# Performance work log

Hardware: AMD Instinct MI355X
Metric: run time of the kernel (lower is better)

## Reference

```python
import jax, jax.numpy as jnp
import numpy as np


def setup_inputs() -> dict:
    key = jax.random.key(0)
    k1, k2 = jax.random.split(key)
    z_e_x = jax.random.normal(k1, (4096, 16, 128), dtype=jnp.float32)
    codebook = jax.random.normal(k2, (1024, 128), dtype=jnp.float32)
    return {"z_e_x": z_e_x, "codebook": codebook}


def reference(z_e_x, codebook):
    # VQStraightThrough.forward: nearest-codebook quantization in fp32.
    B, N, C = z_e_x.shape
    x = z_e_x.astype(jnp.float32).reshape(B * N, C)          # [BN, C]
    cb = codebook.astype(jnp.float32)                        # [K, C]
    inputs_sq = jnp.sum(x * x, axis=1, keepdims=True)        # [BN, 1]
    codebook_sq = jnp.sum(cb * cb, axis=1)                   # [K]
    l2_dis = inputs_sq + codebook_sq - 2.0 * (x @ cb.T)      # [BN, K]
    flat_idx = jnp.argmin(l2_dis, axis=1)                    # [BN] int
    min_vals = jnp.min(l2_dis, axis=1)                       # [BN]
    idx = flat_idx.reshape(B, N)
    distances = min_vals.reshape(B, N).astype(z_e_x.dtype)
    codes = cb[flat_idx].reshape(B, N, C).astype(z_e_x.dtype)  # gather
    return codes, flat_idx, idx, distances
```

## Files before the change

### kernel.cpp

```cpp
#include <hip/hip_runtime.h>
#include <math.h>
#include <stdint.h>

#define C        128
#define KCODES   1024
#define TPB      256
#define ROWS_PB  128
#define NCHUNK   64
#define NCHUNKS  (KCODES / NCHUNK)
#define BSTRIDE  272
#define EPS_TRIG 0.25f

typedef __attribute__((ext_vector_type(8))) short bf16x8_t;
typedef __attribute__((ext_vector_type(4))) float f32x4_t;

static __device__ __forceinline__ uint32_t bf16_rne(float f) {
    uint32_t u = __float_as_uint(f);
    return (u + 0x7FFFu + ((u >> 16) & 1u)) >> 16;
}
static __device__ __forceinline__ float bf16_hi_f(float f) {
    return __uint_as_float(bf16_rne(f) << 16);
}

__global__ void cb_split_kernel(const float* __restrict__ cb,
                                uint16_t* __restrict__ cbh,
                                uint16_t* __restrict__ cbl) {
    int i = blockIdx.x * blockDim.x + threadIdx.x;
    if (i >= KCODES * C) return;
    float f = cb[i];
    uint32_t h = bf16_rne(f);
    float lo = f - __uint_as_float(h << 16);
    cbh[i] = (uint16_t)h;
    cbl[i] = (uint16_t)bf16_rne(lo);
}

__global__ void cbsq_kernel(const float* __restrict__ cb, float* __restrict__ cbsq) {
    const int k = blockIdx.x * blockDim.x + threadIdx.x;
    if (k >= KCODES) return;
    const float4* cp = (const float4*)(cb + (size_t)k * C);
    float sx = 0.f, sy = 0.f, sz = 0.f, sw = 0.f;
    #pragma unroll
    for (int i = 0; i < C / 4; ++i) {
        float4 v = cp[i];
        sx += v.x * v.x; sy += v.y * v.y;
        sz += v.z * v.z; sw += v.w * v.w;
    }
    cbsq[k] = (sx + sy) + (sz + sw);
}

#define SLOTS(OP) OP(0,0) OP(0,1) OP(0,2) OP(0,3) OP(1,0) OP(1,1) OP(1,2) OP(1,3)
#define MFMA_BF16 __builtin_amdgcn_mfma_f32_16x16x32_bf16

__global__ __launch_bounds__(TPB, 3)
void vq_mfma_kernel(const float* __restrict__ x,
                    const float* __restrict__ cb,
                    const uint16_t* __restrict__ cbh,
                    const uint16_t* __restrict__ cbl,
                    const float* __restrict__ cq,
                    float* __restrict__ out_codes,
                    float* __restrict__ out_fidx,
                    float* __restrict__ out_idx,
                    float* __restrict__ out_dist,
                    int rows)
{
    __shared__ __align__(16) uint8_t s_buf[NCHUNK * 2 * BSTRIDE];
    __shared__ float s_cq[NCHUNK];
    __shared__ float s_v1[ROWS_PB], s_v2[ROWS_PB];
    __shared__ int   s_k1[ROWS_PB], s_k2[ROWS_PB];

    const int t    = threadIdx.x;
    const int lane = t & 63;
    const int w    = t >> 6;
    const int ln   = lane & 15;
    const int quad = lane >> 4;
    const int rowblock = blockIdx.x * ROWS_PB;

    #pragma unroll 4
    for (int i = 0; i < 16; ++i) {
        int fid = t + i * TPB;
        int row = fid >> 5;
        int kq  = fid & 31;
        int grow = rowblock + row;
        grow = grow < rows ? grow : rows - 1;
        float4 v = ((const float4*)x)[(size_t)grow * 32 + kq];
        uint32_t p0 = bf16_rne(v.x) | (bf16_rne(v.y) << 16);
        uint32_t p1 = bf16_rne(v.z) | (bf16_rne(v.w) << 16);
        *(uint2*)(s_buf + row * BSTRIDE + kq * 8) = make_uint2(p0, p1);
    }
    __syncthreads();

    const int arow0 = (w * 32 + ln) * BSTRIDE;
    const int arow1 = (w * 32 + 16 + ln) * BSTRIDE;
    bf16x8_t ah00, ah01, ah02, ah03, ah10, ah11, ah12, ah13;
    ah00 = *(const bf16x8_t*)(s_buf + arow0 + 0 * 64 + quad * 16);
    ah01 = *(const bf16x8_t*)(s_buf + arow0 + 1 * 64 + quad * 16);
    ah02 = *(const bf16x8_t*)(s_buf + arow0 + 2 * 64 + quad * 16);
    ah03 = *(const bf16x8_t*)(s_buf + arow0 + 3 * 64 + quad * 16);
    ah10 = *(const bf16x8_t*)(s_buf + arow1 + 0 * 64 + quad * 16);
    ah11 = *(const bf16x8_t*)(s_buf + arow1 + 1 * 64 + quad * 16);
    ah12 = *(const bf16x8_t*)(s_buf + arow1 + 2 * 64 + quad * 16);
    ah13 = *(const bf16x8_t*)(s_buf + arow1 + 3 * 64 + quad * 16);
    __syncthreads();

    #pragma unroll 4
    for (int i = 0; i < 16; ++i) {
        int fid = t + i * TPB;
        int row = fid >> 5;
        int kq  = fid & 31;
        int grow = rowblock + row;
        grow = grow < rows ? grow : rows - 1;
        float4 v = ((const float4*)x)[(size_t)grow * 32 + kq];
        uint32_t p0 = bf16_rne(v.x - bf16_hi_f(v.x)) | (bf16_rne(v.y - bf16_hi_f(v.y)) << 16);
        uint32_t p1 = bf16_rne(v.z - bf16_hi_f(v.z)) | (bf16_rne(v.w - bf16_hi_f(v.w)) << 16);
        *(uint2*)(s_buf + row * BSTRIDE + kq * 8) = make_uint2(p0, p1);
    }
    __syncthreads();

    bf16x8_t al00, al01, al02, al03, al10, al11, al12, al13;
    al00 = *(const bf16x8_t*)(s_buf + arow0 + 0 * 64 + quad * 16);
    al01 = *(const bf16x8_t*)(s_buf + arow0 + 1 * 64 + quad * 16);
    al02 = *(const bf16x8_t*)(s_buf + arow0 + 2 * 64 + quad * 16);
    al03 = *(const bf16x8_t*)(s_buf + arow0 + 3 * 64 + quad * 16);
    al10 = *(const bf16x8_t*)(s_buf + arow1 + 0 * 64 + quad * 16);
    al11 = *(const bf16x8_t*)(s_buf + arow1 + 1 * 64 + quad * 16);
    al12 = *(const bf16x8_t*)(s_buf + arow1 + 2 * 64 + quad * 16);
    al13 = *(const bf16x8_t*)(s_buf + arow1 + 3 * 64 + quad * 16);
    __syncthreads();

#define DECL(g,r) float v1_##g##r = INFINITY, v2_##g##r = INFINITY; int k1_##g##r = 0, k2_##g##r = 0;
    SLOTS(DECL)
#undef DECL

    #pragma unroll 1
    for (int chn = 0; chn < NCHUNKS; ++chn) {
        const int kbase = chn * NCHUNK;
        #pragma unroll
        for (int i = 0; i < 4; ++i) {
            int uid  = t + i * TPB;
            int code = uid >> 4, g = uid & 15;
            uint4 dh = ((const uint4*)cbh)[(size_t)(kbase + code) * 16 + g];
            *(uint4*)(s_buf + code * BSTRIDE + g * 16) = dh;
            uint4 dl = ((const uint4*)cbl)[(size_t)(kbase + code) * 16 + g];
            *(uint4*)(s_buf + NCHUNK * BSTRIDE + code * BSTRIDE + g * 16) = dl;
        }
        if (t < NCHUNK) s_cq[t] = cq[kbase + t];
        __syncthreads();

        const uint8_t* bbase  = s_buf + (size_t)ln * BSTRIDE + quad * 16;
        #pragma unroll
        for (int ct = 0; ct < 4; ++ct) {
            const uint8_t* bh_p = bbase + (size_t)ct * 16 * BSTRIDE;
            const uint8_t* bl_p = bh_p + NCHUNK * BSTRIDE;
            f32x4_t acc0 = {0.f, 0.f, 0.f, 0.f};
            f32x4_t acc1 = {0.f, 0.f, 0.f, 0.f};
#define KSTEP(kk) { \
            bf16x8_t bh = *(const bf16x8_t*)(bh_p + kk * 64); \
            bf16x8_t bl = *(const bf16x8_t*)(bl_p + kk * 64); \
            acc0 = MFMA_BF16(ah0##kk, bh, acc0, 0, 0, 0); \
            acc0 = MFMA_BF16(al0##kk, bh, acc0, 0, 0, 0); \
            acc0 = MFMA_BF16(ah0##kk, bl, acc0, 0, 0, 0); \
            acc1 = MFMA_BF16(ah1##kk, bh, acc1, 0, 0, 0); \
            acc1 = MFMA_BF16(al1##kk, bh, acc1, 0, 0, 0); \
            acc1 = MFMA_BF16(ah1##kk, bl, acc1, 0, 0, 0); }
            KSTEP(0) KSTEP(1) KSTEP(2) KSTEP(3)
#undef KSTEP
            const float cqv = s_cq[ct * 16 + ln];
            const int   kc  = kbase + ct * 16 + ln;
#define UPD(g,r) { \
            float s_ = fmaf(-2.0f, (g ? acc1 : acc0)[r], cqv); \
            bool c1_ = s_ < v1_##g##r; \
            bool c2_ = s_ < v2_##g##r; \
            v2_##g##r = c1_ ? v1_##g##r : (c2_ ? s_ : v2_##g##r); \
            k2_##g##r = c1_ ? k1_##g##r : (c2_ ? kc : k2_##g##r); \
            v1_##g##r = c1_ ? s_ : v1_##g##r; \
            k1_##g##r = c1_ ? kc : k1_##g##r; }
            SLOTS(UPD)
#undef UPD
        }
        __syncthreads();
    }

    for (int m_ = 1; m_ <= 8; m_ <<= 1) {
#define MRG(g,r) { \
        float ov1 = __shfl_xor(v1_##g##r, m_, 16); int ok1 = __shfl_xor(k1_##g##r, m_, 16); \
        float ov2 = __shfl_xor(v2_##g##r, m_, 16); int ok2 = __shfl_xor(k2_##g##r, m_, 16); \
        if (ov1 < v1_##g##r || (ov1 == v1_##g##r && ok1 < k1_##g##r)) { \
            if (v1_##g##r < ov2 || (v1_##g##r == ov2 && k1_##g##r < ok2)) { v2_##g##r = v1_##g##r; k2_##g##r = k1_##g##r; } \
            else { v2_##g##r = ov2; k2_##g##r = ok2; } \
            v1_##g##r = ov1; k1_##g##r = ok1; \
        } else if (ov1 < v2_##g##r || (ov1 == v2_##g##r && ok1 < k2_##g##r)) { \
            v2_##g##r = ov1; k2_##g##r = ok1; \
        } }
        SLOTS(MRG)
#undef MRG
    }
    if (ln == 0) {
#define WRT(g,r) { int rloc = w * 32 + g * 16 + quad * 4 + r; \
        s_v1[rloc] = v1_##g##r; s_v2[rloc] = v2_##g##r; \
        s_k1[rloc] = k1_##g##r; s_k2[rloc] = k2_##g##r; }
        SLOTS(WRT)
#undef WRT
    }
    __syncthreads();

    if (t < ROWS_PB) {
        int rowg = rowblock + t;
        const bool valid = rowg < rows;
        rowg = valid ? rowg : rows - 1;
        float v1 = s_v1[t], v2 = s_v2[t];
        int k1 = s_k1[t], k2 = s_k2[t];
        const float* xr = x + (size_t)rowg * C;

        float sx = 0.f, sy = 0.f, sz = 0.f, sw = 0.f;
        {
            const float4* xp = (const float4*)xr;
            #pragma unroll
            for (int i = 0; i < C / 4; ++i) {
                float4 v = xp[i];
                sx += v.x * v.x; sy += v.y * v.y;
                sz += v.z * v.z; sw += v.w * v.w;
            }
        }
        const float rs = (sx + sy) + (sz + sw);

        bool switched = false;
        double qwin = 0.0;
        if (v2 - v1 < EPS_TRIG) {
            const float* c1p = cb + (size_t)k1 * C;
            const float* c2p = cb + (size_t)k2 * C;
            double dot1 = 0.0, cq1 = 0.0, dot2 = 0.0, cq2 = 0.0;
            #pragma unroll 8
            for (int c = 0; c < C; ++c) {
                const double xc  = (double)xr[c];
                const double cv1 = (double)c1p[c];
                const double cv2 = (double)c2p[c];
                dot1 += xc * cv1;  cq1 += cv1 * cv1;
                dot2 += xc * cv2;  cq2 += cv2 * cv2;
            }
            const double q1 = cq1 - 2.0 * dot1;
            const double q2 = cq2 - 2.0 * dot2;
            if (q2 < q1 || (q2 == q1 && k2 < k1)) { k1 = k2; switched = true; qwin = q2; }
        }

        const float* c1p = cb + (size_t)k1 * C;
        float a = 0.f;
        #pragma unroll 16
        for (int c = 0; c < C; ++c) a = fmaf(xr[c], c1p[c], a);
        float d = (rs + cq[k1]) - 2.f * a;
        if (switched) d = (float)((double)rs + qwin);

        if (valid) {
            out_fidx[rowg] = (float)k1;
            out_idx[rowg]  = (float)k1;
            out_dist[rowg] = d;
        }
        s_k1[t] = k1;
    }
    __syncthreads();

    {
        const int r    = t >> 1;
        const int half = t & 1;
        const int rowg = rowblock + r;
        if (rowg < rows) {
            const int k1 = s_k1[r];
            const float4* src = (const float4*)(cb + (size_t)k1 * C) + half * 16;
            float4*       dst = (float4*)(out_codes + (size_t)rowg * C) + half * 16;
            #pragma unroll
            for (int i = 0; i < 16; ++i) dst[i] = src[i];
        }
    }
}

__global__ __launch_bounds__(TPB, 1)
void vq_nearest_fallback(const float* __restrict__ x,
                         const float* __restrict__ cb,
                         float* __restrict__ out_codes,
                         float* __restrict__ out_fidx,
                         float* __restrict__ out_idx,
                         float* __restrict__ out_dist,
                         int rows)
{
    __shared__ float s_cbsq[KCODES];
    const int t = threadIdx.x;
    for (int k = t; k < KCODES; k += TPB) {
        const float4* cp = (const float4*)(cb + (size_t)k * C);
        float sx = 0.f, sy = 0.f, sz = 0.f, sw = 0.f;
        #pragma unroll
        for (int i = 0; i < C / 4; ++i) {
            float4 v = cp[i];
            sx += v.x * v.x; sy += v.y * v.y; sz += v.z * v.z; sw += v.w * v.w;
        }
        s_cbsq[k] = (sx + sy) + (sz + sw);
    }
    __syncthreads();
    const int row = blockIdx.x * TPB + t;
    if (row >= rows) return;
    float xr[C];
    {
        const float4* xp = (const float4*)(x + (size_t)row * C);
        #pragma unroll
        for (int i = 0; i < C / 4; ++i) {
            float4 v = xp[i];
            xr[4*i+0] = v.x; xr[4*i+1] = v.y; xr[4*i+2] = v.z; xr[4*i+3] = v.w;
        }
    }
    float rs;
    {
        float sx = 0.f, sy = 0.f, sz = 0.f, sw = 0.f;
        #pragma unroll
        for (int i = 0; i < C / 4; ++i) {
            sx += xr[4*i+0]*xr[4*i+0]; sy += xr[4*i+1]*xr[4*i+1];
            sz += xr[4*i+2]*xr[4*i+2]; sw += xr[4*i+3]*xr[4*i+3];
        }
        rs = (sx + sy) + (sz + sw);
    }
    float v1 = INFINITY, v2 = INFINITY; int k1 = 0, k2 = 0;
    #pragma unroll 1
    for (int k0 = 0; k0 < KCODES; k0 += 4) {
        const float* c0 = cb + (size_t)k0 * C;
        float a0 = 0.f, a1 = 0.f, a2 = 0.f, a3 = 0.f;
        #pragma unroll
        for (int c = 0; c < C; ++c) {
            const float xc = xr[c];
            a0 = fmaf(xc, c0[c], a0);
            a1 = fmaf(xc, c0[C + c], a1);
            a2 = fmaf(xc, c0[2*C + c], a2);
            a3 = fmaf(xc, c0[3*C + c], a3);
        }
        const float d0 = (rs + s_cbsq[k0+0]) - 2.f * a0;
        const float d1 = (rs + s_cbsq[k0+1]) - 2.f * a1;
        const float d2 = (rs + s_cbsq[k0+2]) - 2.f * a2;
        const float d3 = (rs + s_cbsq[k0+3]) - 2.f * a3;
        #define UPDF(dv, ki)                                                 \
            if ((dv) < v1)      { v2 = v1; k2 = k1; v1 = (dv); k1 = (ki); } \
            else if ((dv) < v2) { v2 = (dv); k2 = (ki); }
        UPDF(d0, k0+0); UPDF(d1, k0+1); UPDF(d2, k0+2); UPDF(d3, k0+3);
        #undef UPDF
    }
    if (v2 - v1 < 0.125f) {
        const float* c1p = cb + (size_t)k1 * C;
        const float* c2p = cb + (size_t)k2 * C;
        double dot1 = 0.0, cq1 = 0.0, dot2 = 0.0, cq2 = 0.0;
        #pragma unroll 8
        for (int c = 0; c < C; ++c) {
            const double xc = (double)xr[c];
            const double cv1 = (double)c1p[c];
            const double cv2 = (double)c2p[c];
            dot1 += xc * cv1; cq1 += cv1 * cv1;
            dot2 += xc * cv2; cq2 += cv2 * cv2;
        }
        const double q1 = cq1 - 2.0 * dot1;
        const double q2 = cq2 - 2.0 * dot2;
        if (q2 < q1 || (q2 == q1 && k2 < k1)) { k1 = k2; v1 = (float)((double)rs + q2); }
    }
    {
        const float4* src = (const float4*)(cb + (size_t)k1 * C);
        float4* dst = (float4*)(out_codes + (size_t)row * C);
        #pragma unroll
        for (int i = 0; i < C / 4; ++i) dst[i] = src[i];
        out_fidx[row] = (float)k1;
        out_idx[row]  = (float)k1;
        out_dist[row] = v1;
    }
}

extern "C" void kernel_launch(void* const* d_in, const int* in_sizes, int n_in,
                              void* d_out, int out_size, void* d_ws, size_t ws_size,
                              hipStream_t stream) {
    const float* x  = (const float*)d_in[0];
    const float* cb = (const float*)d_in[1];
    const int rows = in_sizes[0] / C;

    float* out       = (float*)d_out;
    float* out_codes = out;
    float* out_fidx  = out + (size_t)rows * C;
    float* out_idx   = out_fidx + rows;
    float* out_dist  = out_idx + rows;

    const size_t cbh_off = 0;
    const size_t cbl_off = (size_t)KCODES * C * sizeof(uint16_t);
    const size_t cq_off  = cbl_off * 2;
    const size_t need    = cq_off + KCODES * sizeof(float);

    if (ws_size >= need) {
        uint16_t* cbh = (uint16_t*)((char*)d_ws + cbh_off);
        uint16_t* cbl = (uint16_t*)((char*)d_ws + cbl_off);
        float*    cq  = (float*)((char*)d_ws + cq_off);

        cb_split_kernel<<<(KCODES * C + TPB - 1) / TPB, TPB, 0, stream>>>(cb, cbh, cbl);
        cbsq_kernel<<<(KCODES + TPB - 1) / TPB, TPB, 0, stream>>>(cb, cq);

        const int grid = (rows + ROWS_PB - 1) / ROWS_PB;
        vq_mfma_kernel<<<grid, TPB, 0, stream>>>(x, cb, cbh, cbl, cq,
                                                 out_codes, out_fidx, out_idx,
                                                 out_dist, rows);
    } else {
        const int rowblocks = (rows + TPB - 1) / TPB;
        vq_nearest_fallback<<<rowblocks, TPB, 0, stream>>>(x, cb, out_codes, out_fidx,
                                                           out_idx, out_dist, rows);
    }
}
```

Measured before the change: 174.7 us.

## Double-buffer codebook chunks via register prefetch and fuse codebook prep kernels

Codebook hi/lo chunks and their squared norms are now prefetched into registers for the next chunk while MFMAs run on the current one, then written into a second LDS buffer. This drops one barrier per chunk and hides the global load latency. LDS usage doubles to about 70KB per block, so occupancy bound falls from 3 to 2 blocks per CU and register pressure rises. The split and norm kernels are also merged into one launch.

```diff
diff --git a/kernel.cpp b/kernel.cpp
--- a/kernel.cpp
+++ b/kernel.cpp
@@ -9,6 +9,8 @@
 #define NCHUNK   64
 #define NCHUNKS  (KCODES / NCHUNK)
 #define BSTRIDE  272
+#define BHALF    (NCHUNK * BSTRIDE)
+#define BUFBYTES (2 * BHALF)
 #define EPS_TRIG 0.25f
 
 typedef __attribute__((ext_vector_type(8))) short bf16x8_t;
@@ -22,36 +24,35 @@
     return __uint_as_float(bf16_rne(f) << 16);
 }
 
-__global__ void cb_split_kernel(const float* __restrict__ cb,
-                                uint16_t* __restrict__ cbh,
-                                uint16_t* __restrict__ cbl) {
-    int i = blockIdx.x * blockDim.x + threadIdx.x;
-    if (i >= KCODES * C) return;
-    float f = cb[i];
-    uint32_t h = bf16_rne(f);
-    float lo = f - __uint_as_float(h << 16);
-    cbh[i] = (uint16_t)h;
-    cbl[i] = (uint16_t)bf16_rne(lo);
-}
-
-__global__ void cbsq_kernel(const float* __restrict__ cb, float* __restrict__ cbsq) {
-    const int k = blockIdx.x * blockDim.x + threadIdx.x;
-    if (k >= KCODES) return;
-    const float4* cp = (const float4*)(cb + (size_t)k * C);
-    float sx = 0.f, sy = 0.f, sz = 0.f, sw = 0.f;
-    #pragma unroll
-    for (int i = 0; i < C / 4; ++i) {
-        float4 v = cp[i];
-        sx += v.x * v.x; sy += v.y * v.y;
-        sz += v.z * v.z; sw += v.w * v.w;
-    }
-    cbsq[k] = (sx + sy) + (sz + sw);
+__global__ void cb_prep_kernel(const float* __restrict__ cb,
+                               uint16_t* __restrict__ cbh,
+                               uint16_t* __restrict__ cbl,
+                               float* __restrict__ cbsq) {
+    const int i = blockIdx.x * blockDim.x + threadIdx.x;
+    if (i < KCODES * C) {
+        float f = cb[i];
+        uint32_t h = bf16_rne(f);
+        float lo = f - __uint_as_float(h << 16);
+        cbh[i] = (uint16_t)h;
+        cbl[i] = (uint16_t)bf16_rne(lo);
+    }
+    if (i < KCODES) {
+        const float4* cp = (const float4*)(cb + (size_t)i * C);
+        float sx = 0.f, sy = 0.f, sz = 0.f, sw = 0.f;
+        #pragma unroll
+        for (int j = 0; j < C / 4; ++j) {
+            float4 v = cp[j];
+            sx += v.x * v.x; sy += v.y * v.y;
+            sz += v.z * v.z; sw += v.w * v.w;
+        }
+        cbsq[i] = (sx + sy) + (sz + sw);
+    }
 }
 
 #define SLOTS(OP) OP(0,0) OP(0,1) OP(0,2) OP(0,3) OP(1,0) OP(1,1) OP(1,2) OP(1,3)
 #define MFMA_BF16 __builtin_amdgcn_mfma_f32_16x16x32_bf16
 
-__global__ __launch_bounds__(TPB, 3)
+__global__ __launch_bounds__(TPB, 2)
 void vq_mfma_kernel(const float* __restrict__ x,
                     const float* __restrict__ cb,
                     const uint16_t* __restrict__ cbh,
@@ -63,8 +64,8 @@
                     float* __restrict__ out_dist,
                     int rows)
 {
-    __shared__ __align__(16) uint8_t s_buf[NCHUNK * 2 * BSTRIDE];
-    __shared__ float s_cq[NCHUNK];
+    __shared__ __align__(16) uint8_t s_buf[2 * BUFBYTES];
+    __shared__ float s_cq[2][NCHUNK];
     __shared__ float s_v1[ROWS_PB], s_v2[ROWS_PB];
     __shared__ int   s_k1[ROWS_PB], s_k2[ROWS_PB];
 
@@ -74,6 +75,34 @@
     const int ln   = lane & 15;
     const int quad = lane >> 4;
     const int rowblock = blockIdx.x * ROWS_PB;
+
+    const uint4* cbh4 = (const uint4*)cbh;
+    const uint4* cbl4 = (const uint4*)cbl;
+
+    uint4 rh0, rh1, rh2, rh3, rl0, rl1, rl2, rl3;
+    float cqr = 0.f;
+
+#define STAGE_LOAD(chn) { \
+    const size_t gb = (size_t)(chn) * (NCHUNK * 16); \
+    rh0 = cbh4[gb + t + 0 * TPB]; rh1 = cbh4[gb + t + 1 * TPB]; \
+    rh2 = cbh4[gb + t + 2 * TPB]; rh3 = cbh4[gb + t + 3 * TPB]; \
+    rl0 = cbl4[gb + t + 0 * TPB]; rl1 = cbl4[gb + t + 1 * TPB]; \
+    rl2 = cbl4[gb + t + 2 * TPB]; rl3 = cbl4[gb + t + 3 * TPB]; \
+    if (t < NCHUNK) cqr = cq[(chn) * NCHUNK + t]; }
+
+#define STAGE_WRITE(bi) { \
+    uint8_t* sb = s_buf + (bi) * BUFBYTES; \
+    { int uid = t + 0 * TPB; uint8_t* p = sb + (uid >> 4) * BSTRIDE + (uid & 15) * 16; \
+      *(uint4*)p = rh0; *(uint4*)(p + BHALF) = rl0; } \
+    { int uid = t + 1 * TPB; uint8_t* p = sb + (uid >> 4) * BSTRIDE + (uid & 15) * 16; \
+      *(uint4*)p = rh1; *(uint4*)(p + BHALF) = rl1; } \
+    { int uid = t + 2 * TPB; uint8_t* p = sb + (uid >> 4) * BSTRIDE + (uid & 15) * 16; \
+      *(uint4*)p = rh2; *(uint4*)(p + BHALF) = rl2; } \
+    { int uid = t + 3 * TPB; uint8_t* p = sb + (uid >> 4) * BSTRIDE + (uid & 15) * 16; \
+      *(uint4*)p = rh3; *(uint4*)(p + BHALF) = rl3; } \
+    if (t < NCHUNK) s_cq[bi][t] = cqr; }
+
+    STAGE_LOAD(0);
 
     #pragma unroll 4
     for (int i = 0; i < 16; ++i) {
@@ -127,30 +156,25 @@
     al13 = *(const bf16x8_t*)(s_buf + arow1 + 3 * 64 + quad * 16);
     __syncthreads();
 
+    STAGE_WRITE(0);
+    __syncthreads();
+
 #define DECL(g,r) float v1_##g##r = INFINITY, v2_##g##r = INFINITY; int k1_##g##r = 0, k2_##g##r = 0;
     SLOTS(DECL)
 #undef DECL
 
     #pragma unroll 1
     for (int chn = 0; chn < NCHUNKS; ++chn) {
+        const int buf   = chn & 1;
         const int kbase = chn * NCHUNK;
-        #pragma unroll
-        for (int i = 0; i < 4; ++i) {
-            int uid  = t + i * TPB;
-            int code = uid >> 4, g = uid & 15;
-            uint4 dh = ((const uint4*)cbh)[(size_t)(kbase + code) * 16 + g];
-            *(uint4*)(s_buf + code * BSTRIDE + g * 16) = dh;
-            uint4 dl = ((const uint4*)cbl)[(size_t)(kbase + code) * 16 + g];
-            *(uint4*)(s_buf + NCHUNK * BSTRIDE + code * BSTRIDE + g * 16) = dl;
-        }
-        if (t < NCHUNK) s_cq[t] = cq[kbase + t];
-        __syncthreads();
-
-        const uint8_t* bbase  = s_buf + (size_t)ln * BSTRIDE + quad * 16;
+
+        if (chn + 1 < NCHUNKS) STAGE_LOAD(chn + 1);
+
+        const uint8_t* bbase = s_buf + buf * BUFBYTES + (size_t)ln * BSTRIDE + quad * 16;
         #pragma unroll
         for (int ct = 0; ct < 4; ++ct) {
             const uint8_t* bh_p = bbase + (size_t)ct * 16 * BSTRIDE;
-            const uint8_t* bl_p = bh_p + NCHUNK * BSTRIDE;
+            const uint8_t* bl_p = bh_p + BHALF;
             f32x4_t acc0 = {0.f, 0.f, 0.f, 0.f};
             f32x4_t acc1 = {0.f, 0.f, 0.f, 0.f};
 #define KSTEP(kk) { \
@@ -164,7 +188,7 @@
             acc1 = MFMA_BF16(ah1##kk, bl, acc1, 0, 0, 0); }
             KSTEP(0) KSTEP(1) KSTEP(2) KSTEP(3)
 #undef KSTEP
-            const float cqv = s_cq[ct * 16 + ln];
+            const float cqv = s_cq[buf][ct * 16 + ln];
             const int   kc  = kbase + ct * 16 + ln;
 #define UPD(g,r) { \
             float s_ = fmaf(-2.0f, (g ? acc1 : acc0)[r], cqv); \
@@ -177,6 +201,8 @@
             SLOTS(UPD)
 #undef UPD
         }
+
+        if (chn + 1 < NCHUNKS) STAGE_WRITE(buf ^ 1);
         __syncthreads();
     }
 
@@ -270,6 +296,8 @@
             for (int i = 0; i < 16; ++i) dst[i] = src[i];
         }
     }
+#undef STAGE_LOAD
+#undef STAGE_WRITE
 }
 
 __global__ __launch_bounds__(TPB, 1)
@@ -388,8 +416,7 @@
         uint16_t* cbl = (uint16_t*)((char*)d_ws + cbl_off);
         float*    cq  = (float*)((char*)d_ws + cq_off);
 
-        cb_split_kernel<<<(KCODES * C + TPB - 1) / TPB, TPB, 0, stream>>>(cb, cbh, cbl);
-        cbsq_kernel<<<(KCODES + TPB - 1) / TPB, TPB, 0, stream>>>(cb, cq);
+        cb_prep_kernel<<<(KCODES * C + TPB - 1) / TPB, TPB, 0, stream>>>(cb, cbh, cbl, cq);
 
         const int grid = (rows + ROWS_PB - 1) / ROWS_PB;
         vq_mfma_kernel<<<grid, TPB, 0, stream>>>(x, cb, cbh, cbl, cq,
```

After: 164.6 us. 5.8% less time.

## Split codebook search across two blocks per row tile and add finalize kernel

Applied to the files above, without the earlier changes.

The main MFMA kernel now processes only half of the codebook per block, so the grid doubles. Each block writes a per-row top-2 (value, index) record to workspace. A separate finalize kernel merges the two halves, runs the fp32/fp64 refinement and writes the gathered codes. The two codebook prep kernels are fused into one launch. The aim is more blocks for better occupancy and load balance on the GPU, paid for by an extra launch, global top-2 traffic, and reloading and re-converting the x tile in both half-blocks.

```diff
diff --git a/kernel.cpp b/kernel.cpp
--- a/kernel.cpp
+++ b/kernel.cpp
@@ -4,11 +4,13 @@
 
 #define C        128
 #define KCODES   1024
+#define KHALF    512
 #define TPB      256
 #define ROWS_PB  128
 #define NCHUNK   64
-#define NCHUNKS  (KCODES / NCHUNK)
+#define NCHUNKS_H (KHALF / NCHUNK)
 #define BSTRIDE  272
+#define BHALF    (NCHUNK * BSTRIDE)
 #define EPS_TRIG 0.25f
 
 typedef __attribute__((ext_vector_type(8))) short bf16x8_t;
@@ -22,58 +24,54 @@
     return __uint_as_float(bf16_rne(f) << 16);
 }
 
-__global__ void cb_split_kernel(const float* __restrict__ cb,
-                                uint16_t* __restrict__ cbh,
-                                uint16_t* __restrict__ cbl) {
-    int i = blockIdx.x * blockDim.x + threadIdx.x;
-    if (i >= KCODES * C) return;
-    float f = cb[i];
-    uint32_t h = bf16_rne(f);
-    float lo = f - __uint_as_float(h << 16);
-    cbh[i] = (uint16_t)h;
-    cbl[i] = (uint16_t)bf16_rne(lo);
-}
-
-__global__ void cbsq_kernel(const float* __restrict__ cb, float* __restrict__ cbsq) {
-    const int k = blockIdx.x * blockDim.x + threadIdx.x;
-    if (k >= KCODES) return;
-    const float4* cp = (const float4*)(cb + (size_t)k * C);
-    float sx = 0.f, sy = 0.f, sz = 0.f, sw = 0.f;
-    #pragma unroll
-    for (int i = 0; i < C / 4; ++i) {
-        float4 v = cp[i];
-        sx += v.x * v.x; sy += v.y * v.y;
-        sz += v.z * v.z; sw += v.w * v.w;
-    }
-    cbsq[k] = (sx + sy) + (sz + sw);
+__global__ void cb_prep_kernel(const float* __restrict__ cb,
+                               uint16_t* __restrict__ cbh,
+                               uint16_t* __restrict__ cbl,
+                               float* __restrict__ cbsq) {
+    const int i = blockIdx.x * blockDim.x + threadIdx.x;
+    if (i < KCODES * C) {
+        float f = cb[i];
+        uint32_t h = bf16_rne(f);
+        float lo = f - __uint_as_float(h << 16);
+        cbh[i] = (uint16_t)h;
+        cbl[i] = (uint16_t)bf16_rne(lo);
+    }
+    if (i < KCODES) {
+        const float4* cp = (const float4*)(cb + (size_t)i * C);
+        float sx = 0.f, sy = 0.f, sz = 0.f, sw = 0.f;
+        #pragma unroll
+        for (int j = 0; j < C / 4; ++j) {
+            float4 v = cp[j];
+            sx += v.x * v.x; sy += v.y * v.y;
+            sz += v.z * v.z; sw += v.w * v.w;
+        }
+        cbsq[i] = (sx + sy) + (sz + sw);
+    }
 }
 
 #define SLOTS(OP) OP(0,0) OP(0,1) OP(0,2) OP(0,3) OP(1,0) OP(1,1) OP(1,2) OP(1,3)
 #define MFMA_BF16 __builtin_amdgcn_mfma_f32_16x16x32_bf16
 
-__global__ __launch_bounds__(TPB, 3)
-void vq_mfma_kernel(const float* __restrict__ x,
-                    const float* __restrict__ cb,
-                    const uint16_t* __restrict__ cbh,
-                    const uint16_t* __restrict__ cbl,
-                    const float* __restrict__ cq,
-                    float* __restrict__ out_codes,
-                    float* __restrict__ out_fidx,
-                    float* __restrict__ out_idx,
-                    float* __restrict__ out_dist,
-                    int rows)
+__global__ __launch_bounds__(TPB, 4)
+void vq_partial_kernel(const float* __restrict__ x,
+                       const uint16_t* __restrict__ cbh,
+                       const uint16_t* __restrict__ cbl,
+                       const float* __restrict__ cq,
+                       float4* __restrict__ top2,
+                       int rows)
 {
-    __shared__ __align__(16) uint8_t s_buf[NCHUNK * 2 * BSTRIDE];
+    __shared__ __align__(16) uint8_t s_buf[2 * BHALF];
     __shared__ float s_cq[NCHUNK];
-    __shared__ float s_v1[ROWS_PB], s_v2[ROWS_PB];
-    __shared__ int   s_k1[ROWS_PB], s_k2[ROWS_PB];
 
     const int t    = threadIdx.x;
     const int lane = t & 63;
     const int w    = t >> 6;
     const int ln   = lane & 15;
     const int quad = lane >> 4;
-    const int rowblock = blockIdx.x * ROWS_PB;
+    const int rb   = blockIdx.x >> 1;
+    const int kh   = blockIdx.x & 1;
+    const int rowblock = rb * ROWS_PB;
+    const int kh0      = kh * KHALF;
 
     #pragma unroll 4
     for (int i = 0; i < 16; ++i) {
@@ -132,8 +130,8 @@
 #undef DECL
 
     #pragma unroll 1
-    for (int chn = 0; chn < NCHUNKS; ++chn) {
-        const int kbase = chn * NCHUNK;
+    for (int chn = 0; chn < NCHUNKS_H; ++chn) {
+        const int kbase = kh0 + chn * NCHUNK;
         #pragma unroll
         for (int i = 0; i < 4; ++i) {
             int uid  = t + i * TPB;
@@ -141,16 +139,16 @@
             uint4 dh = ((const uint4*)cbh)[(size_t)(kbase + code) * 16 + g];
             *(uint4*)(s_buf + code * BSTRIDE + g * 16) = dh;
             uint4 dl = ((const uint4*)cbl)[(size_t)(kbase + code) * 16 + g];
-            *(uint4*)(s_buf + NCHUNK * BSTRIDE + code * BSTRIDE + g * 16) = dl;
+            *(uint4*)(s_buf + BHALF + code * BSTRIDE + g * 16) = dl;
         }
         if (t < NCHUNK) s_cq[t] = cq[kbase + t];
         __syncthreads();
 
-        const uint8_t* bbase  = s_buf + (size_t)ln * BSTRIDE + quad * 16;
+        const uint8_t* bbase = s_buf + (size_t)ln * BSTRIDE + quad * 16;
         #pragma unroll
         for (int ct = 0; ct < 4; ++ct) {
             const uint8_t* bh_p = bbase + (size_t)ct * 16 * BSTRIDE;
-            const uint8_t* bl_p = bh_p + NCHUNK * BSTRIDE;
+            const uint8_t* bl_p = bh_p + BHALF;
             f32x4_t acc0 = {0.f, 0.f, 0.f, 0.f};
             f32x4_t acc1 = {0.f, 0.f, 0.f, 0.f};
 #define KSTEP(kk) { \
@@ -196,19 +194,53 @@
     }
     if (ln == 0) {
 #define WRT(g,r) { int rloc = w * 32 + g * 16 + quad * 4 + r; \
-        s_v1[rloc] = v1_##g##r; s_v2[rloc] = v2_##g##r; \
-        s_k1[rloc] = k1_##g##r; s_k2[rloc] = k2_##g##r; }
+        int rowg = rowblock + rloc; \
+        if (rowg < rows) { \
+            top2[(size_t)kh * rows + rowg] = \
+                make_float4(v1_##g##r, __int_as_float(k1_##g##r), \
+                            v2_##g##r, __int_as_float(k2_##g##r)); } }
         SLOTS(WRT)
 #undef WRT
     }
-    __syncthreads();
-
-    if (t < ROWS_PB) {
-        int rowg = rowblock + t;
+}
+
+#define FROWS 64
+
+__global__ __launch_bounds__(TPB, 4)
+void vq_finalize_kernel(const float* __restrict__ x,
+                        const float* __restrict__ cb,
+                        const float* __restrict__ cq,
+                        const float4* __restrict__ top2,
+                        float* __restrict__ out_codes,
+                        float* __restrict__ out_fidx,
+                        float* __restrict__ out_idx,
+                        float* __restrict__ out_dist,
+                        int rows)
+{
+    __shared__ int s_k1[FROWS];
+    const int t    = threadIdx.x;
+    const int base = blockIdx.x * FROWS;
+
+    if (t < FROWS) {
+        int rowg = base + t;
         const bool valid = rowg < rows;
         rowg = valid ? rowg : rows - 1;
-        float v1 = s_v1[t], v2 = s_v2[t];
-        int k1 = s_k1[t], k2 = s_k2[t];
+
+        float4 ha = top2[rowg];
+        float4 hb = top2[(size_t)rows + rowg];
+        float av1 = ha.x, av2 = ha.z;  int ak1 = __float_as_int(ha.y), ak2 = __float_as_int(ha.w);
+        float bv1 = hb.x, bv2 = hb.z;  int bk1 = __float_as_int(hb.y), bk2 = __float_as_int(hb.w);
+        float v1, v2; int k1, k2;
+        if (bv1 < av1 || (bv1 == av1 && bk1 < ak1)) {
+            v1 = bv1; k1 = bk1;
+            if (av1 < bv2 || (av1 == bv2 && ak1 < bk2)) { v2 = av1; k2 = ak1; }
+            else                                        { v2 = bv2; k2 = bk2; }
+        } else {
+            v1 = av1; k1 = ak1;
+            if (bv1 < av2 || (bv1 == av2 && bk1 < ak2)) { v2 = bv1; k2 = bk1; }
+            else                                        { v2 = av2; k2 = ak2; }
+        }
+
         const float* xr = x + (size_t)rowg * C;
 
         float sx = 0.f, sy = 0.f, sz = 0.f, sw = 0.f;
@@ -259,15 +291,15 @@
     __syncthreads();
 
     {
-        const int r    = t >> 1;
-        const int half = t & 1;
-        const int rowg = rowblock + r;
+        const int r   = t >> 2;
+        const int sub = t & 3;
+        const int rowg = base + r;
         if (rowg < rows) {
             const int k1 = s_k1[r];
-            const float4* src = (const float4*)(cb + (size_t)k1 * C) + half * 16;
-            float4*       dst = (float4*)(out_codes + (size_t)rowg * C) + half * 16;
+            const float4* src = (const float4*)(cb + (size_t)k1 * C) + sub * 8;
+            float4*       dst = (float4*)(out_codes + (size_t)rowg * C) + sub * 8;
             #pragma unroll
-            for (int i = 0; i < 16; ++i) dst[i] = src[i];
+            for (int i = 0; i < 8; ++i) dst[i] = src[i];
         }
     }
 }
@@ -378,23 +410,27 @@
     float* out_idx   = out_fidx + rows;
     float* out_dist  = out_idx + rows;
 
-    const size_t cbh_off = 0;
-    const size_t cbl_off = (size_t)KCODES * C * sizeof(uint16_t);
-    const size_t cq_off  = cbl_off * 2;
-    const size_t need    = cq_off + KCODES * sizeof(float);
+    const size_t cbh_off  = 0;
+    const size_t cbl_off  = (size_t)KCODES * C * sizeof(uint16_t);
+    const size_t cq_off   = cbl_off * 2;
+    const size_t top2_off = cq_off + KCODES * sizeof(float);
+    const size_t need     = top2_off + (size_t)2 * rows * sizeof(float4);
 
     if (ws_size >= need) {
-        uint16_t* cbh = (uint16_t*)((char*)d_ws + cbh_off);
-        uint16_t* cbl = (uint16_t*)((char*)d_ws + cbl_off);
-        float*    cq  = (float*)((char*)d_ws + cq_off);
-
-        cb_split_kernel<<<(KCODES * C + TPB - 1) / TPB, TPB, 0, stream>>>(cb, cbh, cbl);
-        cbsq_kernel<<<(KCODES + TPB - 1) / TPB, TPB, 0, stream>>>(cb, cq);
-
-        const int grid = (rows + ROWS_PB - 1) / ROWS_PB;
-        vq_mfma_kernel<<<grid, TPB, 0, stream>>>(x, cb, cbh, cbl, cq,
-                                                 out_codes, out_fidx, out_idx,
-                                                 out_dist, rows);
+        uint16_t* cbh  = (uint16_t*)((char*)d_ws + cbh_off);
+        uint16_t* cbl  = (uint16_t*)((char*)d_ws + cbl_off);
+        float*    cq   = (float*)((char*)d_ws + cq_off);
+        float4*   top2 = (float4*)((char*)d_ws + top2_off);
+
+        cb_prep_kernel<<<(KCODES * C + TPB - 1) / TPB, TPB, 0, stream>>>(cb, cbh, cbl, cq);
+
+        const int rowblocks = (rows + ROWS_PB - 1) / ROWS_PB;
+        vq_partial_kernel<<<rowblocks * 2, TPB, 0, stream>>>(x, cbh, cbl, cq, top2, rows);
+
+        const int fblocks = (rows + FROWS - 1) / FROWS;
+        vq_finalize_kernel<<<fblocks, TPB, 0, stream>>>(x, cb, cq, top2,
+                                                        out_codes, out_fidx,
+                                                        out_idx, out_dist, rows);
     } else {
         const int rowblocks = (rows + TPB - 1) / TPB;
         vq_nearest_fallback<<<rowblocks, TPB, 0, stream>>>(x, cb, out_codes, out_fidx,
```

Measured after the change: 286.9 us. +64.2%, slower.
